# Optimization experiments

Measured on AMD Instinct MI355X. Metric: run time of the kernel, lower is better.

The kernel has to match this reference:

```python
import jax, jax.numpy as jnp
import numpy as np
import math

HIDDEN_DIM = 1024
NUM_MODALITIES = 8
NUM_HEADS = 8
HEAD_DIM = HIDDEN_DIM // NUM_HEADS
LN_EPS = 1e-5


def setup_inputs() -> dict:
    key = jax.random.key(0)
    ks = jax.random.split(key, 12)
    B, K, D = 8192, NUM_MODALITIES, HIDDEN_DIM
    s = 1.0 / math.sqrt(D)
    inp = {
        'modality_encodings': jax.random.normal(ks[0], (B, K, D), dtype=jnp.float32),
        'selection_mask': jnp.ones((B, K), dtype=jnp.float32),
        # nn.Linear weights are [out, in]
        'wq': jax.random.uniform(ks[1], (D, D), jnp.float32, -s, s),
        'bq': jax.random.uniform(ks[2], (D,), jnp.float32, -s, s),
        'wk': jax.random.uniform(ks[3], (D, D), jnp.float32, -s, s),
        'bk': jax.random.uniform(ks[4], (D,), jnp.float32, -s, s),
        'wv': jax.random.uniform(ks[5], (D, D), jnp.float32, -s, s),
        'bv': jax.random.uniform(ks[6], (D,), jnp.float32, -s, s),
        'wo': jax.random.uniform(ks[7], (D, D), jnp.float32, -s, s),
        'bo': jax.random.uniform(ks[8], (D,), jnp.float32, -s, s),
        'rel_prior': jnp.eye(K, dtype=jnp.float32) + 0.1 * jax.random.normal(ks[9], (K, K), dtype=jnp.float32),
        'ln_gamma': jnp.ones((D,), dtype=jnp.float32),
        'ln_beta': jnp.zeros((D,), dtype=jnp.float32),
    }
    return inp


def reference(modality_encodings, selection_mask, wq, bq, wk, bk, wv, bv, wo, bo,
              rel_prior, ln_gamma, ln_beta):
    x = modality_encodings  # [B, K, D]
    B, K, D = x.shape
    H, Hd = NUM_HEADS, HEAD_DIM

    def lin(t, w, b):
        return t @ w.T + b

    def heads(t):  # [B,K,D] -> [B,H,K,Hd]
        return t.reshape(B, K, H, Hd).transpose(0, 2, 1, 3)

    q = heads(lin(x, wq, bq))
    k = heads(lin(x, wk, bk))
    v = heads(lin(x, wv, bv))

    scores = jnp.einsum('bhqd,bhkd->bhqk', q, k) / math.sqrt(Hd)
    scores = scores + rel_prior[None, None, :, :]  # learned additive bias

    # selection mask: mask_2d[b,q,k] = mask[b,q]*mask[b,k]; fill -inf where 0
    mask_2d = (selection_mask[:, :, None] * selection_mask[:, None, :]) > 0  # [B,K,K]
    scores = jnp.where(mask_2d[:, None, :, :], scores, -jnp.inf)

    attn = jax.nn.softmax(scores, axis=-1)
    # dropout(p=0.1) in eval mode -> identity
    out = jnp.einsum('bhqk,bhkd->bhqd', attn, v)  # [B,H,K,Hd]
    out = out.transpose(0, 2, 1, 3).reshape(B, K, D)
    out = lin(out, wo, bo)

    res = x + out
    mu = jnp.mean(res, axis=-1, keepdims=True)
    var = jnp.mean(jnp.square(res - mu), axis=-1, keepdims=True)
    return (res - mu) * jax.lax.rsqrt(var + LN_EPS) * ln_gamma + ln_beta
```

## Files before the change

### kernel.cpp

```cpp
#include <hip/hip_runtime.h>

typedef __attribute__((ext_vector_type(4))) float f32x4;
typedef __attribute__((ext_vector_type(8))) short short8;

#define LN_EPS 1e-5f

__device__ __forceinline__ float bf2f(short x) {
  union { unsigned u; float f; } c;
  c.u = ((unsigned)(unsigned short)x) << 16;
  return c.f;
}
__device__ __forceinline__ short f2b(float f) {
  union { float f; unsigned u; } c; c.f = f;
  unsigned r = (c.u + 0x7fffu + ((c.u >> 16) & 1u)) >> 16;
  return (short)r;
}

__global__ __launch_bounds__(256) void cvt_kernel(const float* __restrict__ src,
                                                  short* __restrict__ dst, int n8) {
  int idx = blockIdx.x * 256 + threadIdx.x;
  int stride = gridDim.x * 256;
  for (int c = idx; c < n8; c += stride) {
    const f32x4* s = (const f32x4*)(src + (size_t)c * 8);
    f32x4 v0 = s[0], v1 = s[1];
    short8 o;
    o[0] = f2b(v0.x); o[1] = f2b(v0.y); o[2] = f2b(v0.z); o[3] = f2b(v0.w);
    o[4] = f2b(v1.x); o[5] = f2b(v1.y); o[6] = f2b(v1.z); o[7] = f2b(v1.w);
    *(short8*)(dst + (size_t)c * 8) = o;
  }
}

__global__ __launch_bounds__(256) void pack_bias(const float* __restrict__ bq,
                                                 const float* __restrict__ bk,
                                                 const float* __restrict__ bv,
                                                 float* __restrict__ dst) {
  int t = blockIdx.x * 256 + threadIdx.x;
  if (t < 1024) { dst[t] = bq[t]; dst[1024 + t] = bk[t]; dst[2048 + t] = bv[t]; }
}

__device__ __forceinline__ void gload16(const short* g, const short* l) {
  __builtin_amdgcn_global_load_lds((const __attribute__((address_space(1))) unsigned int*)g,
                                   (__attribute__((address_space(3))) unsigned int*)l,
                                   16, 0, 0);
}

template <int MODE>
__global__ __launch_bounds__(512, 2) void gemm256(
    const short* __restrict__ A, const short* __restrict__ W,
    const float* __restrict__ bias, const float* __restrict__ resid,
    void* __restrict__ Cptr, int N) {
  __shared__ __align__(16) short lds[65536];

  const int tid = threadIdx.x;
  const int w = tid >> 6, l = tid & 63;
  const int wr = w >> 2, wc = w & 3;
  const int r0 = l & 15, hk = l >> 4;

  const int q = gridDim.x >> 3;
  const int wg = (blockIdx.x & 7) * q + (blockIdx.x >> 3);
  const int nbx = N >> 8;
  const int mb = wg / nbx, nb = wg - mb * nbx;
  const int m0 = mb << 8, n0 = nb << 8;

  const int srow = tid >> 2;
  const int slot = (tid & 3) ^ (srow & 3);
  const short* gA0 = A + (size_t)(m0 + srow) * 1024 + slot * 8;
  const short* gA1 = gA0 + (size_t)128 * 1024;
  const short* gB0 = W + (size_t)(n0 + srow) * 1024 + slot * 8;
  const short* gB1 = gB0 + (size_t)128 * 1024;

  const int fslot = (hk ^ (r0 & 3)) * 8;
  const int aoff = (wr * 128 + r0) * 32 + fslot;
  const int boff = (wc * 64 + r0) * 32 + fslot;

  f32x4 acc[8][4];
#pragma unroll
  for (int i = 0; i < 8; ++i)
#pragma unroll
    for (int j = 0; j < 4; ++j) acc[i][j] = (f32x4)(0.f);

#pragma unroll
  for (int u = 0; u < 3; ++u) {
    short* Ab = &lds[u * 16384];
    short* Bb = &lds[u * 16384 + 8192];
    gload16(gA0 + u * 32, Ab + w * 512);
    gload16(gA1 + u * 32, Ab + 4096 + w * 512);
    gload16(gB0 + u * 32, Bb + w * 512);
    gload16(gB1 + u * 32, Bb + 4096 + w * 512);
  }

#pragma unroll 4
  for (int t = 0; t < 32; ++t) {
    __builtin_amdgcn_sched_barrier(0);
    if (t < 30)      { asm volatile("s_waitcnt vmcnt(8)" ::: "memory"); }
    else if (t == 30){ asm volatile("s_waitcnt vmcnt(4)" ::: "memory"); }
    else             { asm volatile("s_waitcnt vmcnt(0)" ::: "memory"); }
    __builtin_amdgcn_s_barrier();
    __builtin_amdgcn_sched_barrier(0);

    const int buf = t & 3;
    const short* Ab = &lds[buf * 16384];
    const short* Bb = &lds[buf * 16384 + 8192];
    short8 av[8], bw[4];
#pragma unroll
    for (int i = 0; i < 8; ++i) av[i] = *(const short8*)&Ab[aoff + i * 512];
#pragma unroll
    for (int j = 0; j < 4; ++j) bw[j] = *(const short8*)&Bb[boff + j * 512];

    if (t < 29) {
      const int u = t + 3, b2 = u & 3;
      short* A2 = &lds[b2 * 16384];
      short* B2 = &lds[b2 * 16384 + 8192];
      gload16(gA0 + u * 32, A2 + w * 512);
      gload16(gA1 + u * 32, A2 + 4096 + w * 512);
      gload16(gB0 + u * 32, B2 + w * 512);
      gload16(gB1 + u * 32, B2 + 4096 + w * 512);
    }

    __builtin_amdgcn_s_setprio(1);
#pragma unroll
    for (int i = 0; i < 8; ++i)
#pragma unroll
      for (int j = 0; j < 4; ++j)
        acc[i][j] = __builtin_amdgcn_mfma_f32_16x16x32_bf16(av[i], bw[j], acc[i][j], 0, 0, 0);
    __builtin_amdgcn_s_setprio(0);
  }

  const int crow = m0 + wr * 128 + hk * 4;
  const int ccol = n0 + wc * 64 + r0;
  if (MODE == 0) {
    short* C = (short*)Cptr;
#pragma unroll
    for (int j = 0; j < 4; ++j) {
      float bj = bias[ccol + j * 16];
#pragma unroll
      for (int i = 0; i < 8; ++i) {
        size_t base = (size_t)(crow + i * 16) * N + (ccol + j * 16);
#pragma unroll
        for (int rr = 0; rr < 4; ++rr)
          C[base + (size_t)rr * N] = f2b(acc[i][j][rr] + bj);
      }
    }
  } else {
    float* C = (float*)Cptr;
#pragma unroll
    for (int j = 0; j < 4; ++j) {
      float bj = bias[ccol + j * 16];
#pragma unroll
      for (int i = 0; i < 8; ++i) {
        size_t base = (size_t)(crow + i * 16) * N + (ccol + j * 16);
#pragma unroll
        for (int rr = 0; rr < 4; ++rr)
          C[base + (size_t)rr * N] =
              acc[i][j][rr] + bj + resid[base + (size_t)rr * N];
      }
    }
  }
}

__global__ __launch_bounds__(256) void attn_kernel(
    const short* __restrict__ qkv, const float* __restrict__ prior,
    const float* __restrict__ mask, short* __restrict__ out) {
  __shared__ short sq[8 * 3080];
  const int tid = threadIdx.x;
  const int b = blockIdx.x;
  for (int c = tid; c < 3072; c += 256) {
    int row = c / 384;
    int cc = c - row * 384;
    *(short8*)&sq[row * 3080 + cc * 8] =
        *(const short8*)&qkv[((size_t)b * 8 + row) * 3072 + cc * 8];
  }
  __syncthreads();
  const int l = tid & 63, w = tid >> 6;
  const int i = l >> 3, j = l & 7;
  const float pv = prior[l];
  const float mm = mask[b * 8 + i] * mask[b * 8 + j];
#pragma unroll
  for (int hh = 0; hh < 2; ++hh) {
    const int h = w + hh * 4;
    const short* Qr = &sq[i * 3080 + h * 128];
    const short* Kr = &sq[j * 3080 + 1024 + h * 128];
    float s = 0.f;
#pragma unroll
    for (int c = 0; c < 16; ++c) {
      short8 qa = *(const short8*)&Qr[c * 8];
      short8 ka = *(const short8*)&Kr[c * 8];
#pragma unroll
      for (int e = 0; e < 8; ++e) s += bf2f(qa[e]) * bf2f(ka[e]);
    }
    s = s * 0.08838834764831843f + pv;
    if (!(mm > 0.f)) s = -__builtin_inff();
    float mx = s;
#pragma unroll
    for (int off = 1; off < 8; off <<= 1) mx = fmaxf(mx, __shfl_xor(mx, off));
    float e = __expf(s - mx);
    float sum = e;
#pragma unroll
    for (int off = 1; off < 8; off <<= 1) sum += __shfl_xor(sum, off);
    float p = e / sum;
    float o[16];
#pragma unroll
    for (int t = 0; t < 16; ++t) o[t] = 0.f;
#pragma unroll
    for (int jj = 0; jj < 8; ++jj) {
      float pj = __shfl(p, i * 8 + jj);
      const short* Vr = &sq[jj * 3080 + 2048 + h * 128 + j * 16];
      short8 v0 = *(const short8*)&Vr[0];
      short8 v1 = *(const short8*)&Vr[8];
#pragma unroll
      for (int e2 = 0; e2 < 8; ++e2) {
        o[e2] += pj * bf2f(v0[e2]);
        o[8 + e2] += pj * bf2f(v1[e2]);
      }
    }
    short8 o0, o1;
#pragma unroll
    for (int e2 = 0; e2 < 8; ++e2) { o0[e2] = f2b(o[e2]); o1[e2] = f2b(o[8 + e2]); }
    short* dst = out + ((size_t)(b * 8 + i)) * 1024 + h * 128 + j * 16;
    *(short8*)dst = o0;
    *(short8*)(dst + 8) = o1;
  }
}

__global__ __launch_bounds__(256) void ln_kernel(float* __restrict__ io,
                                                 const float* __restrict__ gamma,
                                                 const float* __restrict__ beta) {
  const int l = threadIdx.x & 63, w = threadIdx.x >> 6;
  float* p = io + ((size_t)blockIdx.x * 4 + w) * 1024;
  f32x4 v[4];
  float s = 0.f;
#pragma unroll
  for (int c = 0; c < 4; ++c) {
    v[c] = *(const f32x4*)(p + (c * 64 + l) * 4);
    s += v[c][0] + v[c][1] + v[c][2] + v[c][3];
  }
#pragma unroll
  for (int off = 32; off > 0; off >>= 1) s += __shfl_xor(s, off);
  const float mu = s * (1.f / 1024.f);
  float s2 = 0.f;
#pragma unroll
  for (int c = 0; c < 4; ++c)
#pragma unroll
    for (int e = 0; e < 4; ++e) { float d = v[c][e] - mu; s2 += d * d; }
#pragma unroll
  for (int off = 32; off > 0; off >>= 1) s2 += __shfl_xor(s2, off);
  const float rstd = rsqrtf(s2 * (1.f / 1024.f) + LN_EPS);
#pragma unroll
  for (int c = 0; c < 4; ++c) {
    f32x4 g = *(const f32x4*)(gamma + (c * 64 + l) * 4);
    f32x4 bt = *(const f32x4*)(beta + (c * 64 + l) * 4);
    f32x4 ov;
#pragma unroll
    for (int e = 0; e < 4; ++e) ov[e] = (v[c][e] - mu) * rstd * g[e] + bt[e];
    *(f32x4*)(p + (c * 64 + l) * 4) = ov;
  }
}

extern "C" void kernel_launch(void* const* d_in, const int* in_sizes, int n_in,
                              void* d_out, int out_size, void* d_ws, size_t ws_size,
                              hipStream_t stream) {
  const float* x     = (const float*)d_in[0];
  const float* mask  = (const float*)d_in[1];
  const float* wq    = (const float*)d_in[2];
  const float* bq    = (const float*)d_in[3];
  const float* wk    = (const float*)d_in[4];
  const float* bk    = (const float*)d_in[5];
  const float* wv    = (const float*)d_in[6];
  const float* bv    = (const float*)d_in[7];
  const float* wo    = (const float*)d_in[8];
  const float* bo    = (const float*)d_in[9];
  const float* prior = (const float*)d_in[10];
  const float* gamma = (const float*)d_in[11];
  const float* beta  = (const float*)d_in[12];

  char* ws = (char*)d_ws;
  short* qkv  = (short*)(ws);
  short* xb   = (short*)(ws + 402653184L);
  short* wall = (short*)(ws + 536870912L);
  short* wob  = (short*)(ws + 543162368L);
  float* ball = (float*)(ws + 545259520L);

  cvt_kernel<<<2048, 256, 0, stream>>>(x, xb, 8388608);
  cvt_kernel<<<512, 256, 0, stream>>>(wq, wall,           131072);
  cvt_kernel<<<512, 256, 0, stream>>>(wk, wall + 1048576, 131072);
  cvt_kernel<<<512, 256, 0, stream>>>(wv, wall + 2097152, 131072);
  cvt_kernel<<<512, 256, 0, stream>>>(wo, wob,            131072);
  pack_bias<<<4, 256, 0, stream>>>(bq, bk, bv, ball);

  gemm256<0><<<3072, 512, 0, stream>>>(xb, wall, ball, nullptr, qkv, 3072);
  attn_kernel<<<8192, 256, 0, stream>>>(qkv, prior, mask, xb);
  gemm256<1><<<1024, 512, 0, stream>>>(xb, wob, bo, x, d_out, 1024);
  ln_kernel<<<16384, 256, 0, stream>>>((float*)d_out, gamma, beta);
}
```

Before: 1.049 ms.

## Restructure GEMM main loop into 64-wide K steps with quadrant-phased double buffering

```diff
diff --git a/kernel.cpp b/kernel.cpp
--- a/kernel.cpp
+++ b/kernel.cpp
@@ -56,22 +56,32 @@
   const int wr = w >> 2, wc = w & 3;
   const int r0 = l & 15, hk = l >> 4;
 
-  const int q = gridDim.x >> 3;
-  const int wg = (blockIdx.x & 7) * q + (blockIdx.x >> 3);
+  const int q8 = gridDim.x >> 3;
+  const int wg = (blockIdx.x & 7) * q8 + (blockIdx.x >> 3);
   const int nbx = N >> 8;
   const int mb = wg / nbx, nb = wg - mb * nbx;
   const int m0 = mb << 8, n0 = nb << 8;
 
-  const int srow = tid >> 2;
-  const int slot = (tid & 3) ^ (srow & 3);
-  const short* gA0 = A + (size_t)(m0 + srow) * 1024 + slot * 8;
-  const short* gA1 = gA0 + (size_t)128 * 1024;
-  const short* gB0 = W + (size_t)(n0 + srow) * 1024 + slot * 8;
-  const short* gB1 = gB0 + (size_t)128 * 1024;
-
-  const int fslot = (hk ^ (r0 & 3)) * 8;
-  const int aoff = (wr * 128 + r0) * 32 + fslot;
-  const int boff = (wc * 64 + r0) * 32 + fslot;
+  const int srow = tid >> 3;
+  const int colsh = (((tid & 7) ^ (srow & 7)) << 3);
+  const short* gA00 = A + (size_t)(m0 + srow) * 1024 + colsh;
+  const short* gA01 = A + (size_t)(m0 + srow + 64) * 1024 + colsh;
+  const short* gA10 = A + (size_t)(m0 + 128 + srow) * 1024 + colsh;
+  const short* gA11 = A + (size_t)(m0 + 128 + srow + 64) * 1024 + colsh;
+  const short* gB00 = W + (size_t)(n0 + srow) * 1024 + colsh;
+  const short* gB01 = W + (size_t)(n0 + srow + 64) * 1024 + colsh;
+  const short* gB10 = W + (size_t)(n0 + 128 + srow) * 1024 + colsh;
+  const short* gB11 = W + (size_t)(n0 + 128 + srow + 64) * 1024 + colsh;
+  const int wofs = w * 512;
+
+  const int ps0 = hk ^ (r0 & 7);
+  const int aO0 = r0 * 64 + ps0 * 8;
+  const int aO1 = r0 * 64 + (ps0 ^ 4) * 8;
+  const int rB = (wc & 1) * 64;
+  const int bO0 = (rB + r0) * 64 + ps0 * 8;
+  const int bO1 = (rB + r0) * 64 + (ps0 ^ 4) * 8;
+  const short* Abase = &lds[wr * 8192];
+  const short* Bbase = &lds[32768 + (wc >> 1) * 8192];
 
   f32x4 acc[8][4];
 #pragma unroll
@@ -79,50 +89,102 @@
 #pragma unroll
     for (int j = 0; j < 4; ++j) acc[i][j] = (f32x4)(0.f);
 
-#pragma unroll
-  for (int u = 0; u < 3; ++u) {
-    short* Ab = &lds[u * 16384];
-    short* Bb = &lds[u * 16384 + 8192];
-    gload16(gA0 + u * 32, Ab + w * 512);
-    gload16(gA1 + u * 32, Ab + 4096 + w * 512);
-    gload16(gB0 + u * 32, Bb + w * 512);
-    gload16(gB1 + u * 32, Bb + 4096 + w * 512);
-  }
-
-#pragma unroll 4
-  for (int t = 0; t < 32; ++t) {
-    __builtin_amdgcn_sched_barrier(0);
-    if (t < 30)      { asm volatile("s_waitcnt vmcnt(8)" ::: "memory"); }
-    else if (t == 30){ asm volatile("s_waitcnt vmcnt(4)" ::: "memory"); }
-    else             { asm volatile("s_waitcnt vmcnt(0)" ::: "memory"); }
+  gload16(gA00, &lds[wofs]);
+  gload16(gA01, &lds[wofs + 4096]);
+  gload16(gA10, &lds[8192 + wofs]);
+  gload16(gA11, &lds[8192 + wofs + 4096]);
+  gload16(gB00, &lds[32768 + wofs]);
+  gload16(gB01, &lds[32768 + wofs + 4096]);
+  gload16(gB10, &lds[32768 + 8192 + wofs]);
+  gload16(gB11, &lds[32768 + 8192 + wofs + 4096]);
+
+#pragma unroll 2
+  for (int t = 0; t < 16; ++t) {
+    const int p = t & 1;
+    const short* Ab = Abase + p * 16384;
+    const short* Bb = Bbase + p * 16384;
+    short8 av[4][2], bw[4][2];
+
+    __builtin_amdgcn_sched_barrier(0);
+    asm volatile("s_waitcnt vmcnt(0)" ::: "memory");
     __builtin_amdgcn_s_barrier();
     __builtin_amdgcn_sched_barrier(0);
-
-    const int buf = t & 3;
-    const short* Ab = &lds[buf * 16384];
-    const short* Bb = &lds[buf * 16384 + 8192];
-    short8 av[8], bw[4];
-#pragma unroll
-    for (int i = 0; i < 8; ++i) av[i] = *(const short8*)&Ab[aoff + i * 512];
-#pragma unroll
-    for (int j = 0; j < 4; ++j) bw[j] = *(const short8*)&Bb[boff + j * 512];
-
-    if (t < 29) {
-      const int u = t + 3, b2 = u & 3;
-      short* A2 = &lds[b2 * 16384];
-      short* B2 = &lds[b2 * 16384 + 8192];
-      gload16(gA0 + u * 32, A2 + w * 512);
-      gload16(gA1 + u * 32, A2 + 4096 + w * 512);
-      gload16(gB0 + u * 32, B2 + w * 512);
-      gload16(gB1 + u * 32, B2 + 4096 + w * 512);
-    }
-
+#pragma unroll
+    for (int i4 = 0; i4 < 4; ++i4) {
+      av[i4][0] = *(const short8*)&Ab[aO0 + i4 * 1024];
+      av[i4][1] = *(const short8*)&Ab[aO1 + i4 * 1024];
+    }
+#pragma unroll
+    for (int j = 0; j < 2; ++j) {
+      bw[j][0] = *(const short8*)&Bb[bO0 + j * 1024];
+      bw[j][1] = *(const short8*)&Bb[bO1 + j * 1024];
+    }
+    if (t < 15) {
+      const int kofs = (t + 1) * 64;
+      const int qb = (p ^ 1) * 16384;
+      gload16(gA00 + kofs, &lds[qb + wofs]);
+      gload16(gA01 + kofs, &lds[qb + wofs + 4096]);
+      gload16(gA10 + kofs, &lds[qb + 8192 + wofs]);
+      gload16(gA11 + kofs, &lds[qb + 8192 + wofs + 4096]);
+      gload16(gB00 + kofs, &lds[32768 + qb + wofs]);
+      gload16(gB01 + kofs, &lds[32768 + qb + wofs + 4096]);
+      gload16(gB10 + kofs, &lds[32768 + qb + 8192 + wofs]);
+      gload16(gB11 + kofs, &lds[32768 + qb + 8192 + wofs + 4096]);
+    }
     __builtin_amdgcn_s_setprio(1);
 #pragma unroll
-    for (int i = 0; i < 8; ++i)
-#pragma unroll
-      for (int j = 0; j < 4; ++j)
-        acc[i][j] = __builtin_amdgcn_mfma_f32_16x16x32_bf16(av[i], bw[j], acc[i][j], 0, 0, 0);
+    for (int ks = 0; ks < 2; ++ks)
+#pragma unroll
+      for (int i4 = 0; i4 < 4; ++i4)
+#pragma unroll
+        for (int j = 0; j < 2; ++j)
+          acc[i4][j] = __builtin_amdgcn_mfma_f32_16x16x32_bf16(av[i4][ks], bw[j][ks], acc[i4][j], 0, 0, 0);
+    __builtin_amdgcn_s_setprio(0);
+
+    __builtin_amdgcn_s_barrier();
+    __builtin_amdgcn_sched_barrier(0);
+#pragma unroll
+    for (int j = 2; j < 4; ++j) {
+      bw[j][0] = *(const short8*)&Bb[bO0 + j * 1024];
+      bw[j][1] = *(const short8*)&Bb[bO1 + j * 1024];
+    }
+    __builtin_amdgcn_s_setprio(1);
+#pragma unroll
+    for (int ks = 0; ks < 2; ++ks)
+#pragma unroll
+      for (int i4 = 0; i4 < 4; ++i4)
+#pragma unroll
+        for (int j = 2; j < 4; ++j)
+          acc[i4][j] = __builtin_amdgcn_mfma_f32_16x16x32_bf16(av[i4][ks], bw[j][ks], acc[i4][j], 0, 0, 0);
+    __builtin_amdgcn_s_setprio(0);
+
+    __builtin_amdgcn_s_barrier();
+    __builtin_amdgcn_sched_barrier(0);
+#pragma unroll
+    for (int i4 = 0; i4 < 4; ++i4) {
+      av[i4][0] = *(const short8*)&Ab[aO0 + (4 + i4) * 1024];
+      av[i4][1] = *(const short8*)&Ab[aO1 + (4 + i4) * 1024];
+    }
+    __builtin_amdgcn_s_setprio(1);
+#pragma unroll
+    for (int ks = 0; ks < 2; ++ks)
+#pragma unroll
+      for (int i4 = 0; i4 < 4; ++i4)
+#pragma unroll
+        for (int j = 2; j < 4; ++j)
+          acc[4 + i4][j] = __builtin_amdgcn_mfma_f32_16x16x32_bf16(av[i4][ks], bw[j][ks], acc[4 + i4][j], 0, 0, 0);
+    __builtin_amdgcn_s_setprio(0);
+
+    __builtin_amdgcn_s_barrier();
+    __builtin_amdgcn_sched_barrier(0);
+    __builtin_amdgcn_s_setprio(1);
+#pragma unroll
+    for (int ks = 0; ks < 2; ++ks)
+#pragma unroll
+      for (int i4 = 0; i4 < 4; ++i4)
+#pragma unroll
+        for (int j = 0; j < 2; ++j)
+          acc[4 + i4][j] = __builtin_amdgcn_mfma_f32_16x16x32_bf16(av[i4][ks], bw[j][ks], acc[4 + i4][j], 0, 0, 0);
     __builtin_amdgcn_s_setprio(0);
   }
 
```

New measurement: 1.005 ms. 4.2% less time.

## Restructure GEMM mainloop into 64-wide K tiles with eight-phase interleaved pipeline

Applied to the files above, without the earlier changes.

```diff
diff --git a/kernel.cpp b/kernel.cpp
--- a/kernel.cpp
+++ b/kernel.cpp
@@ -56,22 +56,55 @@
   const int wr = w >> 2, wc = w & 3;
   const int r0 = l & 15, hk = l >> 4;
 
-  const int q = gridDim.x >> 3;
-  const int wg = (blockIdx.x & 7) * q + (blockIdx.x >> 3);
+  const int q8 = gridDim.x >> 3;
+  const int wg = (blockIdx.x & 7) * q8 + (blockIdx.x >> 3);
   const int nbx = N >> 8;
   const int mb = wg / nbx, nb = wg - mb * nbx;
   const int m0 = mb << 8, n0 = nb << 8;
 
-  const int srow = tid >> 2;
-  const int slot = (tid & 3) ^ (srow & 3);
-  const short* gA0 = A + (size_t)(m0 + srow) * 1024 + slot * 8;
-  const short* gA1 = gA0 + (size_t)128 * 1024;
-  const short* gB0 = W + (size_t)(n0 + srow) * 1024 + slot * 8;
-  const short* gB1 = gB0 + (size_t)128 * 1024;
-
-  const int fslot = (hk ^ (r0 & 3)) * 8;
-  const int aoff = (wr * 128 + r0) * 32 + fslot;
-  const int boff = (wc * 64 + r0) * 32 + fslot;
+  const int srow = tid >> 3;
+  const int colsh = (((tid & 7) ^ (srow & 7)) << 3);
+  const short* gA = A + (size_t)(m0 + srow) * 1024 + colsh;
+  const short* gB = W + (size_t)(n0 + srow) * 1024 + colsh;
+  const int wofs = w * 512;
+
+#define STAGE(gbase, ldsbase, half, kt) do {                                   \
+    const short* g_ = (gbase) + (size_t)(half) * 131072 + (size_t)(kt) * 64;   \
+    gload16(g_,         &lds[(ldsbase) + (half) * 8192 + wofs]);               \
+    gload16(g_ + 65536, &lds[(ldsbase) + (half) * 8192 + 4096 + wofs]);        \
+  } while (0)
+
+#define PRE_MFMA_BARRIER() do {                                                \
+    __builtin_amdgcn_sched_barrier(0);                                         \
+    __builtin_amdgcn_s_barrier();                                              \
+    __builtin_amdgcn_sched_barrier(0);                                         \
+    asm volatile("s_waitcnt lgkmcnt(0)" ::: "memory");                         \
+    __builtin_amdgcn_sched_barrier(0);                                         \
+  } while (0)
+
+#define END_BARRIER() do {                                                     \
+    __builtin_amdgcn_sched_barrier(0);                                         \
+    __builtin_amdgcn_s_barrier();                                              \
+    __builtin_amdgcn_sched_barrier(0);                                         \
+  } while (0)
+
+#define MFMA_BLK(AV, B0V, B1V, J0, J1) do {                                    \
+    __builtin_amdgcn_s_setprio(1);                                             \
+    _Pragma("unroll")                                                          \
+    for (int i_ = 0; i_ < 8; ++i_) {                                           \
+      acc[i_][J0] = __builtin_amdgcn_mfma_f32_16x16x32_bf16(AV[i_], B0V, acc[i_][J0], 0, 0, 0); \
+      acc[i_][J1] = __builtin_amdgcn_mfma_f32_16x16x32_bf16(AV[i_], B1V, acc[i_][J1], 0, 0, 0); \
+    }                                                                          \
+    __builtin_amdgcn_s_setprio(0);                                             \
+  } while (0)
+
+#define LDS8(ofs) (*(const short8*)&lds[(ofs)])
+
+  const int swz = r0 & 7;
+  const int ck0 = (hk ^ swz) * 8;
+  const int ck1 = ((hk ^ 4) ^ swz) * 8;
+  const int ar = (wr * 128 + r0) * 64;
+  const int br = 32768 + (wc * 64 + r0) * 64;
 
   f32x4 acc[8][4];
 #pragma unroll
@@ -79,52 +112,99 @@
 #pragma unroll
     for (int j = 0; j < 4; ++j) acc[i][j] = (f32x4)(0.f);
 
-#pragma unroll
-  for (int u = 0; u < 3; ++u) {
-    short* Ab = &lds[u * 16384];
-    short* Bb = &lds[u * 16384 + 8192];
-    gload16(gA0 + u * 32, Ab + w * 512);
-    gload16(gA1 + u * 32, Ab + 4096 + w * 512);
-    gload16(gB0 + u * 32, Bb + w * 512);
-    gload16(gB1 + u * 32, Bb + 4096 + w * 512);
-  }
-
-#pragma unroll 4
-  for (int t = 0; t < 32; ++t) {
-    __builtin_amdgcn_sched_barrier(0);
-    if (t < 30)      { asm volatile("s_waitcnt vmcnt(8)" ::: "memory"); }
-    else if (t == 30){ asm volatile("s_waitcnt vmcnt(4)" ::: "memory"); }
-    else             { asm volatile("s_waitcnt vmcnt(0)" ::: "memory"); }
-    __builtin_amdgcn_s_barrier();
-    __builtin_amdgcn_sched_barrier(0);
-
-    const int buf = t & 3;
-    const short* Ab = &lds[buf * 16384];
-    const short* Bb = &lds[buf * 16384 + 8192];
-    short8 av[8], bw[4];
-#pragma unroll
-    for (int i = 0; i < 8; ++i) av[i] = *(const short8*)&Ab[aoff + i * 512];
-#pragma unroll
-    for (int j = 0; j < 4; ++j) bw[j] = *(const short8*)&Bb[boff + j * 512];
-
-    if (t < 29) {
-      const int u = t + 3, b2 = u & 3;
-      short* A2 = &lds[b2 * 16384];
-      short* B2 = &lds[b2 * 16384 + 8192];
-      gload16(gA0 + u * 32, A2 + w * 512);
-      gload16(gA1 + u * 32, A2 + 4096 + w * 512);
-      gload16(gB0 + u * 32, B2 + w * 512);
-      gload16(gB1 + u * 32, B2 + 4096 + w * 512);
-    }
-
-    __builtin_amdgcn_s_setprio(1);
-#pragma unroll
-    for (int i = 0; i < 8; ++i)
-#pragma unroll
-      for (int j = 0; j < 4; ++j)
-        acc[i][j] = __builtin_amdgcn_mfma_f32_16x16x32_bf16(av[i], bw[j], acc[i][j], 0, 0, 0);
-    __builtin_amdgcn_s_setprio(0);
-  }
+  STAGE(gA, 0, 0, 0);     STAGE(gA, 0, 1, 0);
+  STAGE(gB, 32768, 0, 0); STAGE(gB, 32768, 1, 0);
+  STAGE(gA, 16384, 0, 1); STAGE(gA, 16384, 1, 1);
+  __builtin_amdgcn_sched_barrier(0);
+  asm volatile("s_waitcnt vmcnt(4)" ::: "memory");
+  __builtin_amdgcn_s_barrier();
+  __builtin_amdgcn_sched_barrier(0);
+
+#pragma unroll 1
+  for (int t = 0; t < 8; ++t) {
+    const int kt1 = 2 * t + 1;
+    short8 av0[8], av1[8], bv[2], bw2[2];
+
+#pragma unroll
+    for (int i_ = 0; i_ < 8; ++i_) av0[i_] = LDS8(ar + i_ * 1024 + ck0);
+    bv[0] = LDS8(br + ck0);
+    bv[1] = LDS8(br + 1024 + ck0);
+    STAGE(gB, 49152, 0, kt1);
+    PRE_MFMA_BARRIER();
+    MFMA_BLK(av0, bv[0], bv[1], 0, 1);
+    END_BARRIER();
+
+    bw2[0] = LDS8(br + 2048 + ck0);
+    bw2[1] = LDS8(br + 3072 + ck0);
+#pragma unroll
+    for (int i_ = 0; i_ < 8; ++i_) av1[i_] = LDS8(ar + i_ * 1024 + ck1);
+    STAGE(gB, 49152, 1, kt1);
+    PRE_MFMA_BARRIER();
+    MFMA_BLK(av0, bw2[0], bw2[1], 2, 3);
+    END_BARRIER();
+
+    bv[0] = LDS8(br + ck1);
+    bv[1] = LDS8(br + 1024 + ck1);
+    if (t < 7) STAGE(gA, 0, 0, 2 * t + 2);
+    PRE_MFMA_BARRIER();
+    MFMA_BLK(av1, bv[0], bv[1], 0, 1);
+    END_BARRIER();
+
+    bw2[0] = LDS8(br + 2048 + ck1);
+    bw2[1] = LDS8(br + 3072 + ck1);
+    if (t < 7) {
+      STAGE(gA, 0, 1, 2 * t + 2);
+      __builtin_amdgcn_sched_barrier(0);
+      asm volatile("s_waitcnt vmcnt(4)" ::: "memory");
+    } else {
+      __builtin_amdgcn_sched_barrier(0);
+      asm volatile("s_waitcnt vmcnt(0)" ::: "memory");
+    }
+    PRE_MFMA_BARRIER();
+    MFMA_BLK(av1, bw2[0], bw2[1], 2, 3);
+    END_BARRIER();
+
+#pragma unroll
+    for (int i_ = 0; i_ < 8; ++i_) av0[i_] = LDS8(16384 + ar + i_ * 1024 + ck0);
+    bv[0] = LDS8(16384 + br + ck0);
+    bv[1] = LDS8(16384 + br + 1024 + ck0);
+    if (t < 7) STAGE(gB, 32768, 0, 2 * t + 2);
+    PRE_MFMA_BARRIER();
+    MFMA_BLK(av0, bv[0], bv[1], 0, 1);
+    END_BARRIER();
+
+    bw2[0] = LDS8(16384 + br + 2048 + ck0);
+    bw2[1] = LDS8(16384 + br + 3072 + ck0);
+#pragma unroll
+    for (int i_ = 0; i_ < 8; ++i_) av1[i_] = LDS8(16384 + ar + i_ * 1024 + ck1);
+    if (t < 7) STAGE(gB, 32768, 1, 2 * t + 2);
+    PRE_MFMA_BARRIER();
+    MFMA_BLK(av0, bw2[0], bw2[1], 2, 3);
+    END_BARRIER();
+
+    bv[0] = LDS8(16384 + br + ck1);
+    bv[1] = LDS8(16384 + br + 1024 + ck1);
+    if (t < 7) STAGE(gA, 16384, 0, 2 * t + 3);
+    PRE_MFMA_BARRIER();
+    MFMA_BLK(av1, bv[0], bv[1], 0, 1);
+    END_BARRIER();
+
+    bw2[0] = LDS8(16384 + br + 2048 + ck1);
+    bw2[1] = LDS8(16384 + br + 3072 + ck1);
+    if (t < 7) {
+      STAGE(gA, 16384, 1, 2 * t + 3);
+      __builtin_amdgcn_sched_barrier(0);
+      asm volatile("s_waitcnt vmcnt(4)" ::: "memory");
+    }
+    PRE_MFMA_BARRIER();
+    MFMA_BLK(av1, bw2[0], bw2[1], 2, 3);
+    END_BARRIER();
+  }
+#undef STAGE
+#undef PRE_MFMA_BARRIER
+#undef END_BARRIER
+#undef MFMA_BLK
+#undef LDS8
 
   const int crow = m0 + wr * 128 + hk * 4;
   const int ccol = n0 + wc * 64 + r0;
```

New measurement: 1.515 ms. +44.5%, slower.

## Software-pipeline LDS fragment loads with double-buffered A registers in GEMM

Applied to the files above, without the earlier changes.

```diff
diff --git a/kernel.cpp b/kernel.cpp
--- a/kernel.cpp
+++ b/kernel.cpp
@@ -56,22 +56,60 @@
   const int wr = w >> 2, wc = w & 3;
   const int r0 = l & 15, hk = l >> 4;
 
-  const int q = gridDim.x >> 3;
-  const int wg = (blockIdx.x & 7) * q + (blockIdx.x >> 3);
+  const int q8 = gridDim.x >> 3;
+  const int wg = (blockIdx.x & 7) * q8 + (blockIdx.x >> 3);
   const int nbx = N >> 8;
   const int mb = wg / nbx, nb = wg - mb * nbx;
   const int m0 = mb << 8, n0 = nb << 8;
 
   const int srow = tid >> 2;
-  const int slot = (tid & 3) ^ (srow & 3);
-  const short* gA0 = A + (size_t)(m0 + srow) * 1024 + slot * 8;
-  const short* gA1 = gA0 + (size_t)128 * 1024;
-  const short* gB0 = W + (size_t)(n0 + srow) * 1024 + slot * 8;
-  const short* gB1 = gB0 + (size_t)128 * 1024;
-
-  const int fslot = (hk ^ (r0 & 3)) * 8;
-  const int aoff = (wr * 128 + r0) * 32 + fslot;
-  const int boff = (wc * 64 + r0) * 32 + fslot;
+  const int lcol = (((tid & 3) ^ ((srow >> 1) & 3)) << 3);
+  const short* gA1 = A + (size_t)(m0 + srow) * 1024 + lcol;
+  const short* gA2 = gA1 + 131072;
+  const short* gB1 = W + (size_t)(n0 + srow) * 1024 + lcol;
+  const short* gB2 = gB1 + 131072;
+  const int wofs = w * 512;
+
+#define STAGE(KT) do { const int sl_ = ((KT) & 3) * 16384, ko_ = (KT) * 32;  \
+    gload16(gA1 + ko_, &lds[sl_ + wofs]);                                    \
+    gload16(gA2 + ko_, &lds[sl_ + 4096 + wofs]);                             \
+    gload16(gB1 + ko_, &lds[sl_ + 8192 + wofs]);                             \
+    gload16(gB2 + ko_, &lds[sl_ + 12288 + wofs]); } while (0)
+
+  const int pc = (hk ^ ((r0 >> 1) & 3)) << 3;
+  const int ar = (wr * 128 + r0) * 32 + pc;
+  const int br = 8192 + (wc * 64 + r0) * 32 + pc;
+
+#define LOAD_A(KT, AV) do { const int sb_ = ((KT) & 3) * 16384;              \
+    _Pragma("unroll")                                                        \
+    for (int i_ = 0; i_ < 8; ++i_)                                           \
+      AV[i_] = *(const short8*)&lds[sb_ + ar + i_ * 512]; } while (0)
+
+#define LOAD_B(KT, BV) do { const int sb_ = ((KT) & 3) * 16384;              \
+    _Pragma("unroll")                                                        \
+    for (int j_ = 0; j_ < 4; ++j_)                                           \
+      BV[j_] = *(const short8*)&lds[sb_ + br + j_ * 512]; } while (0)
+
+#define DOMFMA(AV, BV) do { __builtin_amdgcn_s_setprio(1);                   \
+    _Pragma("unroll")                                                        \
+    for (int i_ = 0; i_ < 8; ++i_)                                           \
+      _Pragma("unroll")                                                      \
+      for (int j_ = 0; j_ < 4; ++j_)                                         \
+        acc[i_][j_] = __builtin_amdgcn_mfma_f32_16x16x32_bf16(AV[i_], BV[j_], acc[i_][j_], 0, 0, 0); \
+    __builtin_amdgcn_s_setprio(0); } while (0)
+
+#define ITER(T, CA, NA) do {                                                 \
+    asm volatile("s_waitcnt lgkmcnt(0)" ::: "memory");                       \
+    if ((T) < 29) { STAGE((T) + 3);                                          \
+      asm volatile("s_waitcnt vmcnt(8)" ::: "memory"); }                     \
+    else if ((T) == 29) { asm volatile("s_waitcnt vmcnt(4)" ::: "memory"); } \
+    else { asm volatile("s_waitcnt vmcnt(0)" ::: "memory"); }                \
+    __builtin_amdgcn_s_barrier();                                            \
+    __builtin_amdgcn_sched_barrier(0);                                       \
+    LOAD_B((T), bv);                                                         \
+    if ((T) < 31) LOAD_A((T) + 1, NA);                                       \
+    DOMFMA(CA, bv);                                                          \
+  } while (0)
 
   f32x4 acc[8][4];
 #pragma unroll
@@ -79,52 +117,24 @@
 #pragma unroll
     for (int j = 0; j < 4; ++j) acc[i][j] = (f32x4)(0.f);
 
-#pragma unroll
-  for (int u = 0; u < 3; ++u) {
-    short* Ab = &lds[u * 16384];
-    short* Bb = &lds[u * 16384 + 8192];
-    gload16(gA0 + u * 32, Ab + w * 512);
-    gload16(gA1 + u * 32, Ab + 4096 + w * 512);
-    gload16(gB0 + u * 32, Bb + w * 512);
-    gload16(gB1 + u * 32, Bb + 4096 + w * 512);
-  }
-
-#pragma unroll 4
-  for (int t = 0; t < 32; ++t) {
-    __builtin_amdgcn_sched_barrier(0);
-    if (t < 30)      { asm volatile("s_waitcnt vmcnt(8)" ::: "memory"); }
-    else if (t == 30){ asm volatile("s_waitcnt vmcnt(4)" ::: "memory"); }
-    else             { asm volatile("s_waitcnt vmcnt(0)" ::: "memory"); }
-    __builtin_amdgcn_s_barrier();
-    __builtin_amdgcn_sched_barrier(0);
-
-    const int buf = t & 3;
-    const short* Ab = &lds[buf * 16384];
-    const short* Bb = &lds[buf * 16384 + 8192];
-    short8 av[8], bw[4];
-#pragma unroll
-    for (int i = 0; i < 8; ++i) av[i] = *(const short8*)&Ab[aoff + i * 512];
-#pragma unroll
-    for (int j = 0; j < 4; ++j) bw[j] = *(const short8*)&Bb[boff + j * 512];
-
-    if (t < 29) {
-      const int u = t + 3, b2 = u & 3;
-      short* A2 = &lds[b2 * 16384];
-      short* B2 = &lds[b2 * 16384 + 8192];
-      gload16(gA0 + u * 32, A2 + w * 512);
-      gload16(gA1 + u * 32, A2 + 4096 + w * 512);
-      gload16(gB0 + u * 32, B2 + w * 512);
-      gload16(gB1 + u * 32, B2 + 4096 + w * 512);
-    }
-
-    __builtin_amdgcn_s_setprio(1);
-#pragma unroll
-    for (int i = 0; i < 8; ++i)
-#pragma unroll
-      for (int j = 0; j < 4; ++j)
-        acc[i][j] = __builtin_amdgcn_mfma_f32_16x16x32_bf16(av[i], bw[j], acc[i][j], 0, 0, 0);
-    __builtin_amdgcn_s_setprio(0);
-  }
+  short8 av0[8], av1[8], bv[4];
+
+  STAGE(0); STAGE(1); STAGE(2);
+  asm volatile("s_waitcnt vmcnt(8)" ::: "memory");
+  __builtin_amdgcn_s_barrier();
+  __builtin_amdgcn_sched_barrier(0);
+  LOAD_A(0, av0);
+
+#pragma unroll 1
+  for (int u = 0; u < 16; ++u) {
+    ITER(2 * u,     av0, av1);
+    ITER(2 * u + 1, av1, av0);
+  }
+#undef STAGE
+#undef LOAD_A
+#undef LOAD_B
+#undef DOMFMA
+#undef ITER
 
   const int crow = m0 + wr * 128 + hk * 4;
   const int ccol = n0 + wc * 64 + r0;
```

Measured after the change: 1.042 ms. About the same (-0.7%).
